# Optimization experiments

Hardware: AMD Instinct MI355X
Metric: run time of the kernel (lower is better)

The kernel has to match this reference:

```python
import jax, jax.numpy as jnp
import numpy as np

D_MODEL = 1024
HEADS = 16
DH = D_MODEL // HEADS
ROPE_THETA = 10000.0


def _rope_cache(T, dh, base, dtype):
    half = dh // 2
    inv_freq = 1.0 / (base ** (jnp.arange(half, dtype=dtype) / half))
    t = jnp.arange(T, dtype=dtype)
    freqs = jnp.outer(t, inv_freq)  # [T, half]
    return jnp.sin(freqs), jnp.cos(freqs)


def _apply_rope(x, sin, cos):
    # x: [B, h, T, dh]; sin/cos: [T, dh//2] broadcast over B,h
    half = sin.shape[-1]
    x1, x2 = x[..., :half], x[..., half:2 * half]
    return jnp.concatenate([x1 * cos - x2 * sin, x1 * sin + x2 * cos], axis=-1)


def setup_inputs() -> dict:
    key = jax.random.key(0)
    ks = jax.random.split(key, 5)
    B, T, D = 4, 2048, D_MODEL
    scale = 1.0 / np.sqrt(D)
    x_btd = jax.random.normal(ks[0], (B, T, D), dtype=jnp.float32)
    Wqkv = jax.random.normal(ks[1], (D, 3 * D), dtype=jnp.float32) * scale
    bqkv = jnp.zeros((3 * D,), dtype=jnp.float32)
    Wproj = jax.random.normal(ks[2], (D, D), dtype=jnp.float32) * scale
    bproj = jnp.zeros((D,), dtype=jnp.float32)
    return {"x_btd": x_btd, "Wqkv": Wqkv, "bqkv": bqkv, "Wproj": Wproj, "bproj": bproj}


def reference(x_btd, Wqkv, bqkv, Wproj, bproj):
    B, T, D = x_btd.shape
    h, dh = HEADS, DH
    qkv = x_btd @ Wqkv + bqkv                      # [B, T, 3D]
    q, k, v = jnp.split(qkv, 3, axis=-1)

    def to_heads(z):
        return z.reshape(B, T, h, dh).transpose(0, 2, 1, 3)  # [B, h, T, dh]

    qh, kh, vh = to_heads(q), to_heads(k), to_heads(v)
    sin, cos = _rope_cache(T, dh, ROPE_THETA, x_btd.dtype)
    qh = _apply_rope(qh, sin, cos)
    kh = _apply_rope(kh, sin, cos)

    scores = jnp.einsum('bhqd,bhkd->bhqk', qh, kh) / jnp.sqrt(jnp.asarray(dh, x_btd.dtype))
    attn = jax.nn.softmax(scores, axis=-1)
    out = jnp.einsum('bhqk,bhkd->bhqd', attn, vh)  # [B, h, T, dh]
    out = out.transpose(0, 2, 1, 3).reshape(B, T, D)
    return out @ Wproj + bproj
```

## Files before the change

kernel.cpp:

```cpp
#include <hip/hip_runtime.h>
#include <stdint.h>


typedef float  f32x4  __attribute__((ext_vector_type(4)));
typedef float  f32x16 __attribute__((ext_vector_type(16)));
typedef short  s16x8  __attribute__((ext_vector_type(8)));
typedef unsigned int u32x4 __attribute__((ext_vector_type(4)));
typedef unsigned short u16;
typedef unsigned int   u32;

#define LOG2E 1.4426950408889634f

__device__ __forceinline__ u16 f2bf(float f) {
  u32 u = __float_as_uint(f);
  u32 r = (u + 0x7fffu + ((u >> 16) & 1u)) >> 16;
  return (u16)r;
}

__device__ __forceinline__ u32 cvtpk_bf16(float lo, float hi) {
  u32 w;
  asm("v_cvt_pk_bf16_f32 %0, %1, %2" : "=v"(w) : "v"(lo), "v"(hi));
  return w;
}

__device__ __forceinline__ float fexp2(float x) {
  return __builtin_amdgcn_exp2f(x);
}

__device__ __forceinline__ void gload_lds16(const u16* g, u16* l) {
  __builtin_amdgcn_global_load_lds(
      (const __attribute__((address_space(1))) uint32_t*)g,
      (__attribute__((address_space(3))) uint32_t*)l, 16, 0, 0);
}

__global__ void rope_table_kernel(float* __restrict__ rsin, float* __restrict__ rcos) {
  int idx = blockIdx.x * 256 + threadIdx.x;
  int t = idx >> 5, i = idx & 31;
  float invf = 1.0f / powf(10000.0f, (float)i * (1.0f / 32.0f));
  float ang = (float)t * invf;
  rsin[idx] = sinf(ang);
  rcos[idx] = cosf(ang);
}

__global__ void cvt_bf16_kernel(const float* __restrict__ in, u16* __restrict__ out) {
  int i = blockIdx.x * 256 + threadIdx.x;
  const float4* p = reinterpret_cast<const float4*>(in) + (size_t)i * 2;
  float4 a = p[0], b = p[1];
  u32 w0 = (u32)f2bf(a.x) | ((u32)f2bf(a.y) << 16);
  u32 w1 = (u32)f2bf(a.z) | ((u32)f2bf(a.w) << 16);
  u32 w2 = (u32)f2bf(b.x) | ((u32)f2bf(b.y) << 16);
  u32 w3 = (u32)f2bf(b.z) | ((u32)f2bf(b.w) << 16);
  reinterpret_cast<uint4*>(out)[i] = make_uint4(w0, w1, w2, w3);
}

__global__ void transpose_cvt_kernel(const float* __restrict__ W, u16* __restrict__ Wt,
                                     int rows , int cols ) {
  __shared__ float tile[32][33];
  int k0 = blockIdx.y * 32, n0 = blockIdx.x * 32;
  int t = threadIdx.x;
  int c = t & 31, r0 = t >> 5;
  #pragma unroll
  for (int i = 0; i < 4; i++) {
    int r = r0 + i * 8;
    tile[r][c] = W[(size_t)(k0 + r) * cols + n0 + c];
  }
  __syncthreads();
  int kk = t & 31, nn0 = t >> 5;
  #pragma unroll
  for (int i = 0; i < 4; i++) {
    int nn = nn0 + i * 8;
    Wt[(size_t)(n0 + nn) * rows + k0 + kk] = f2bf(tile[kk][nn]);
  }
}

template<int MODE>
__global__ __launch_bounds__(256) void gemm_kernel(
    const u16* __restrict__ A, const u16* __restrict__ Bt,
    const float* __restrict__ bias,
    const float* __restrict__ rsin, const float* __restrict__ rcos,
    u16* __restrict__ Qg, u16* __restrict__ Kg, u16* __restrict__ Vtg,
    float* __restrict__ Cout, int K)
{
  __shared__ alignas(16) u16 As[128][64];
  __shared__ alignas(16) u16 Bs[128][64];
  int tid = threadIdx.x;
  int lane = tid & 63, wid = tid >> 6;
  int wr = wid >> 1, wc = wid & 1;
  int l15 = lane & 15, lg = lane >> 4;
  int row0 = blockIdx.x * 128, col0 = blockIdx.y * 128;

  f32x4 acc[4][4] = {};

  int sr = lane >> 3, sc = lane & 7;
  int scol = (sc ^ sr) * 8;
  const u16* asrc = A  + (size_t)(row0 + wid * 32 + sr) * K + scol;
  const u16* bsrc = Bt + (size_t)(col0 + wid * 32 + sr) * K + scol;
  u16* aLds = &As[0][0] + wid * 2048;
  u16* bLds = &Bs[0][0] + wid * 2048;

  for (int k0 = 0; k0 < K; k0 += 64) {
    #pragma unroll
    for (int i = 0; i < 4; i++) {
      gload_lds16(asrc + (size_t)(i * 8) * K + k0, aLds + i * 512);
      gload_lds16(bsrc + (size_t)(i * 8) * K + k0, bLds + i * 512);
    }
    __syncthreads();
    #pragma unroll
    for (int kk = 0; kk < 2; kk++) {
      s16x8 af[4], bf[4];
      #pragma unroll
      for (int m = 0; m < 4; m++) {
        int row = wr * 64 + m * 16 + l15;
        int slot = (kk * 4 + lg) ^ (l15 & 7);
        af[m] = *reinterpret_cast<const s16x8*>(&As[row][slot * 8]);
      }
      #pragma unroll
      for (int n = 0; n < 4; n++) {
        int row = wc * 64 + n * 16 + l15;
        int slot = (kk * 4 + lg) ^ (l15 & 7);
        bf[n] = *reinterpret_cast<const s16x8*>(&Bs[row][slot * 8]);
      }
      #pragma unroll
      for (int m = 0; m < 4; m++)
        #pragma unroll
        for (int n = 0; n < 4; n++)
          acc[m][n] = __builtin_amdgcn_mfma_f32_16x16x32_bf16(af[m], bf[n], acc[m][n], 0, 0, 0);
    }
    __syncthreads();
  }

  if (MODE == 0) {
    int wavecol = col0 + wc * 64;
    int sec = wavecol >> 10;
    int h = (wavecol & 1023) >> 6;
    #pragma unroll
    for (int m = 0; m < 4; m++) {
      int rbase = row0 + wr * 64 + m * 16 + lg * 4;
      if (sec < 2) {
        u16* G = (sec == 0) ? Qg : Kg;
        float qs = (sec == 0) ? 0.125f * LOG2E : 1.0f;
        #pragma unroll
        for (int fc = 0; fc < 2; fc++) {
          int dh = fc * 16 + l15;
          float b1 = bias[wavecol + fc * 16 + l15];
          float b2 = bias[wavecol + fc * 16 + l15 + 32];
          #pragma unroll
          for (int j = 0; j < 4; j++) {
            int grow = rbase + j;
            int bidx = grow >> 11, tt = grow & 2047;
            float sn = rsin[tt * 32 + dh], cs = rcos[tt * 32 + dh];
            float v1 = acc[m][fc][j] + b1;
            float v2 = acc[m][fc + 2][j] + b2;
            float lo = (v1 * cs - v2 * sn) * qs;
            float hi = (v1 * sn + v2 * cs) * qs;
            size_t base = ((size_t)(bidx * 16 + h) * 2048 + tt) * 64;
            G[base + dh]      = f2bf(lo);
            G[base + dh + 32] = f2bf(hi);
          }
        }
      } else {
        #pragma unroll
        for (int fc = 0; fc < 4; fc++) {
          int dh = fc * 16 + l15;
          float bb = bias[wavecol + fc * 16 + l15];
          #pragma unroll
          for (int j = 0; j < 4; j++) {
            int grow = rbase + j;
            int bidx = grow >> 11, tt = grow & 2047;
            Vtg[((size_t)(bidx * 16 + h) * 64 + dh) * 2048 + tt] = f2bf(acc[m][fc][j] + bb);
          }
        }
      }
    }
  } else {
    #pragma unroll
    for (int m = 0; m < 4; m++) {
      int grow = row0 + wr * 64 + m * 16 + lg * 4;
      #pragma unroll
      for (int fc = 0; fc < 4; fc++) {
        int col = col0 + wc * 64 + fc * 16 + l15;
        float bb = bias[col];
        #pragma unroll
        for (int j = 0; j < 4; j++)
          Cout[(size_t)(grow + j) * 1024 + col] = acc[m][fc][j] + bb;
      }
    }
  }
}

__global__ __launch_bounds__(256, 4) void attn_kernel(
    const u16* __restrict__ Qg, const u16* __restrict__ Kg, const u16* __restrict__ Vtg,
    u16* __restrict__ Og)
{
  __shared__ alignas(16) u16 Ks[2][4096];
  __shared__ alignas(16) u16 Vs[2][4096];
  int tid = threadIdx.x;
  int lane = tid & 63, wid = tid >> 6;
  int l31 = lane & 31, hi = lane >> 5;
  int bh = blockIdx.x & 63, qt = blockIdx.x >> 6;
  int q = qt * 128 + wid * 32 + l31;
  size_t bh2048 = (size_t)bh * 2048;

  s16x8 aq[4];
  #pragma unroll
  for (int kc = 0; kc < 4; kc++)
    aq[kc] = *reinterpret_cast<const s16x8*>(Qg + (bh2048 + q) * 64 + kc * 16 + hi * 8);

  f32x16 o0 = {}, o1 = {};
  float l_run = 0.f;

  int sr = lane >> 3, sc = lane & 7;
  int scol = (sc ^ sr) * 8;
  const u16* kg0 = Kg  + (bh2048 + wid * 16 + sr) * 64 + scol;
  const u16* kg1 = kg0 + 8 * 64;
  const u16* vg0 = Vtg + ((size_t)bh * 64 + wid * 16 + sr) * 2048 + scol;
  const u16* vg1 = vg0 + 8 * 2048;
  int sdst = wid * 1024;

  int offs[2][4];
  #pragma unroll
  for (int c = 0; c < 2; c++)
    #pragma unroll
    for (int j = 0; j < 4; j++)
      offs[c][j] = (c * 32 + l31) * 64 + (((j * 2 + hi) ^ (l31 & 7)) * 8);

#define STAGE(TT, BUF) do { \
    gload_lds16(kg0 + (size_t)(TT) * 4096, &Ks[BUF][sdst]); \
    gload_lds16(kg1 + (size_t)(TT) * 4096, &Ks[BUF][sdst + 512]); \
    gload_lds16(vg0 + (size_t)(TT) * 64,   &Vs[BUF][sdst]); \
    gload_lds16(vg1 + (size_t)(TT) * 64,   &Vs[BUF][sdst + 512]); \
  } while (0)

#define COMPUTE(B) do { \
    const u16* kb = &Ks[B][0]; \
    const u16* vb = &Vs[B][0]; \
    f32x16 s0 = {}, s1 = {}; \
    __builtin_amdgcn_s_setprio(1); \
    _Pragma("unroll") \
    for (int j = 0; j < 4; j++) { \
      s16x8 kf0 = *reinterpret_cast<const s16x8*>(kb + offs[0][j]); \
      s16x8 kf1 = *reinterpret_cast<const s16x8*>(kb + offs[1][j]); \
      s0 = __builtin_amdgcn_mfma_f32_32x32x16_bf16(kf0, aq[j], s0, 0, 0, 0); \
      s1 = __builtin_amdgcn_mfma_f32_32x32x16_bf16(kf1, aq[j], s1, 0, 0, 0); \
    } \
    __builtin_amdgcn_s_setprio(0); \
    _Pragma("unroll") \
    for (int i = 0; i < 16; i++) { \
      s0[i] = fexp2(s0[i]); \
      s1[i] = fexp2(s1[i]); \
    } \
    float r0 = 0.f, r1 = 0.f, r2 = 0.f, r3 = 0.f; \
    _Pragma("unroll") \
    for (int i = 0; i < 4; i++) { \
      r0 += s0[i] + s0[i + 8]; \
      r1 += s0[i + 4] + s0[i + 12]; \
      r2 += s1[i] + s1[i + 8]; \
      r3 += s1[i + 4] + s1[i + 12]; \
    } \
    float rs = (r0 + r1) + (r2 + r3); \
    rs += __shfl_xor(rs, 32); \
    l_run += rs; \
    s16x8 pf[4]; \
    _Pragma("unroll") \
    for (int ks = 0; ks < 2; ks++) { \
      int rr = ks * 8; \
      u32 a0 = cvtpk_bf16(s0[rr + 0], s0[rr + 1]); \
      u32 b0 = cvtpk_bf16(s0[rr + 4], s0[rr + 5]); \
      u32 a1 = cvtpk_bf16(s0[rr + 2], s0[rr + 3]); \
      u32 b1 = cvtpk_bf16(s0[rr + 6], s0[rr + 7]); \
      asm volatile("v_permlane32_swap_b32 %0, %1" : "+v"(a0), "+v"(b0)); \
      asm volatile("v_permlane32_swap_b32 %0, %1" : "+v"(a1), "+v"(b1)); \
      u32x4 w = {a0, a1, b0, b1}; \
      pf[ks] = __builtin_bit_cast(s16x8, w); \
    } \
    _Pragma("unroll") \
    for (int ks = 0; ks < 2; ks++) { \
      int rr = ks * 8; \
      u32 a0 = cvtpk_bf16(s1[rr + 0], s1[rr + 1]); \
      u32 b0 = cvtpk_bf16(s1[rr + 4], s1[rr + 5]); \
      u32 a1 = cvtpk_bf16(s1[rr + 2], s1[rr + 3]); \
      u32 b1 = cvtpk_bf16(s1[rr + 6], s1[rr + 7]); \
      asm volatile("v_permlane32_swap_b32 %0, %1" : "+v"(a0), "+v"(b0)); \
      asm volatile("v_permlane32_swap_b32 %0, %1" : "+v"(a1), "+v"(b1)); \
      u32x4 w = {a0, a1, b0, b1}; \
      pf[ks + 2] = __builtin_bit_cast(s16x8, w); \
    } \
    __builtin_amdgcn_s_setprio(1); \
    _Pragma("unroll") \
    for (int ks = 0; ks < 4; ks++) { \
      s16x8 vf = *reinterpret_cast<const s16x8*>(vb + offs[0][ks]); \
      o0 = __builtin_amdgcn_mfma_f32_32x32x16_bf16(vf, pf[ks], o0, 0, 0, 0); \
    } \
    _Pragma("unroll") \
    for (int ks = 0; ks < 4; ks++) { \
      s16x8 vf = *reinterpret_cast<const s16x8*>(vb + offs[1][ks]); \
      o1 = __builtin_amdgcn_mfma_f32_32x32x16_bf16(vf, pf[ks], o1, 0, 0, 0); \
    } \
    __builtin_amdgcn_s_setprio(0); \
  } while (0)

  STAGE(0, 0);
  __syncthreads();

  for (int it = 0; it < 16; it++) {
    STAGE(2 * it + 1, 1);
    COMPUTE(0);
    __syncthreads();
    if (it < 15) STAGE(2 * it + 2, 0);
    COMPUTE(1);
    __syncthreads();
  }
#undef STAGE
#undef COMPUTE

  float inv = 1.0f / l_run;
  int b = bh >> 4, h = bh & 15;
  size_t rowbase = ((size_t)b * 2048 + q) * 1024 + h * 64;
  #pragma unroll
  for (int c2 = 0; c2 < 2; c2++) {
    #pragma unroll
    for (int g = 0; g < 4; g++) {
      float e0 = (c2 ? o1[g * 4 + 0] : o0[g * 4 + 0]) * inv;
      float e1 = (c2 ? o1[g * 4 + 1] : o0[g * 4 + 1]) * inv;
      float e2 = (c2 ? o1[g * 4 + 2] : o0[g * 4 + 2]) * inv;
      float e3 = (c2 ? o1[g * 4 + 3] : o0[g * 4 + 3]) * inv;
      u32 w0 = cvtpk_bf16(e0, e1);
      u32 w1 = cvtpk_bf16(e2, e3);
      int d = c2 * 32 + g * 8 + hi * 4;
      uint2 val; val.x = w0; val.y = w1;
      *reinterpret_cast<uint2*>(Og + rowbase + d) = val;
    }
  }
}

extern "C" void kernel_launch(void* const* d_in, const int* in_sizes, int n_in,
                              void* d_out, int out_size, void* d_ws, size_t ws_size,
                              hipStream_t stream) {
  const float* x     = (const float*)d_in[0];
  const float* Wqkv  = (const float*)d_in[1];
  const float* bqkv  = (const float*)d_in[2];
  const float* Wproj = (const float*)d_in[3];
  const float* bproj = (const float*)d_in[4];
  float* out = (float*)d_out;

  char* ws = (char*)d_ws;
  size_t off = 0;
  auto alloc = [&](size_t bytes) {
    void* p = ws + off;
    off += (bytes + 255) & ~(size_t)255;
    return p;
  };
  float* rsin  = (float*)alloc((size_t)2048 * 32 * 4);
  float* rcos  = (float*)alloc((size_t)2048 * 32 * 4);
  u16* xb      = (u16*)alloc((size_t)8192 * 1024 * 2);
  u16* Wqkvt   = (u16*)alloc((size_t)3072 * 1024 * 2);
  u16* Wprojt  = (u16*)alloc((size_t)1024 * 1024 * 2);
  u16* Qg      = (u16*)alloc((size_t)64 * 2048 * 64 * 2);
  u16* Kg      = (u16*)alloc((size_t)64 * 2048 * 64 * 2);
  u16* Vtg     = (u16*)alloc((size_t)64 * 2048 * 64 * 2);
  u16* AOg     = (u16*)alloc((size_t)8192 * 1024 * 2);

  rope_table_kernel<<<256, 256, 0, stream>>>(rsin, rcos);
  cvt_bf16_kernel<<<4096, 256, 0, stream>>>(x, xb);
  transpose_cvt_kernel<<<dim3(96, 32), 256, 0, stream>>>(Wqkv, Wqkvt, 1024, 3072);
  transpose_cvt_kernel<<<dim3(32, 32), 256, 0, stream>>>(Wproj, Wprojt, 1024, 1024);
  gemm_kernel<0><<<dim3(64, 24), 256, 0, stream>>>(xb, Wqkvt, bqkv, rsin, rcos,
                                                   Qg, Kg, Vtg, nullptr, 1024);
  attn_kernel<<<1024, 256, 0, stream>>>(Qg, Kg, Vtg, AOg);
  gemm_kernel<1><<<dim3(64, 8), 256, 0, stream>>>(AOg, Wprojt, bproj, nullptr, nullptr,
                                                  nullptr, nullptr, nullptr, out, 1024);
}
```

Baseline: 201.1 us.

## Add 256x256-tile 8-wave QKV GEMM with double-buffered direct-to-LDS loads

Adds a new QKV projection GEMM kernel that uses 256x256 output tiles, 512 threads and 128 KB of dynamic LDS. It double-buffers the K tiles with direct global-to-LDS loads, interleaves the prefetch with the MFMA phases, and raises wave priority around the MFMAs. The aim is more operand reuse per LDS byte and overlap of memory with compute. The epilogue moves into a shared helper. The launch falls back to the old kernel if the LDS attribute cannot be set, and the grid of 384 blocks is small enough that some CUs may sit idle.

```diff
diff --git a/kernel.cpp b/kernel.cpp
--- a/kernel.cpp
+++ b/kernel.cpp
@@ -70,6 +70,50 @@
   for (int i = 0; i < 4; i++) {
     int nn = nn0 + i * 8;
     Wt[(size_t)(n0 + nn) * rows + k0 + kk] = f2bf(tile[kk][nn]);
+  }
+}
+
+__device__ __forceinline__ void qkv_scatter_frag(
+    int wavecol, int rbase, int l15, f32x4* accm ,
+    const float* bias, const float* rsin, const float* rcos,
+    u16* Qg, u16* Kg, u16* Vtg)
+{
+  int sec = wavecol >> 10;
+  int h = (wavecol & 1023) >> 6;
+  if (sec < 2) {
+    u16* G = (sec == 0) ? Qg : Kg;
+    float qs = (sec == 0) ? 0.125f * LOG2E : 1.0f;
+    #pragma unroll
+    for (int fc = 0; fc < 2; fc++) {
+      int dh = fc * 16 + l15;
+      float b1 = bias[wavecol + fc * 16 + l15];
+      float b2 = bias[wavecol + fc * 16 + l15 + 32];
+      #pragma unroll
+      for (int j = 0; j < 4; j++) {
+        int grow = rbase + j;
+        int bidx = grow >> 11, tt = grow & 2047;
+        float sn = rsin[tt * 32 + dh], cs = rcos[tt * 32 + dh];
+        float v1 = accm[fc][j] + b1;
+        float v2 = accm[fc + 2][j] + b2;
+        float lo = (v1 * cs - v2 * sn) * qs;
+        float hi = (v1 * sn + v2 * cs) * qs;
+        size_t base = ((size_t)(bidx * 16 + h) * 2048 + tt) * 64;
+        G[base + dh]      = f2bf(lo);
+        G[base + dh + 32] = f2bf(hi);
+      }
+    }
+  } else {
+    #pragma unroll
+    for (int fc = 0; fc < 4; fc++) {
+      int dh = fc * 16 + l15;
+      float bb = bias[wavecol + fc * 16 + l15];
+      #pragma unroll
+      for (int j = 0; j < 4; j++) {
+        int grow = rbase + j;
+        int bidx = grow >> 11, tt = grow & 2047;
+        Vtg[((size_t)(bidx * 16 + h) * 64 + dh) * 2048 + tt] = f2bf(accm[fc][j] + bb);
+      }
+    }
   }
 }
 
@@ -131,51 +175,115 @@
 
   if (MODE == 0) {
     int wavecol = col0 + wc * 64;
-    int sec = wavecol >> 10;
-    int h = (wavecol & 1023) >> 6;
     #pragma unroll
     for (int m = 0; m < 4; m++) {
       int rbase = row0 + wr * 64 + m * 16 + lg * 4;
-      if (sec < 2) {
-        u16* G = (sec == 0) ? Qg : Kg;
-        float qs = (sec == 0) ? 0.125f * LOG2E : 1.0f;
-        #pragma unroll
-        for (int fc = 0; fc < 2; fc++) {
-          int dh = fc * 16 + l15;
-          float b1 = bias[wavecol + fc * 16 + l15];
-          float b2 = bias[wavecol + fc * 16 + l15 + 32];
-          #pragma unroll
-          for (int j = 0; j < 4; j++) {
-            int grow = rbase + j;
-            int bidx = grow >> 11, tt = grow & 2047;
-            float sn = rsin[tt * 32 + dh], cs = rcos[tt * 32 + dh];
-            float v1 = acc[m][fc][j] + b1;
-            float v2 = acc[m][fc + 2][j] + b2;
-            float lo = (v1 * cs - v2 * sn) * qs;
-            float hi = (v1 * sn + v2 * cs) * qs;
-            size_t base = ((size_t)(bidx * 16 + h) * 2048 + tt) * 64;
-            G[base + dh]      = f2bf(lo);
-            G[base + dh + 32] = f2bf(hi);
-          }
-        }
-      } else {
-        #pragma unroll
-        for (int fc = 0; fc < 4; fc++) {
-          int dh = fc * 16 + l15;
-          float bb = bias[wavecol + fc * 16 + l15];
-          #pragma unroll
-          for (int j = 0; j < 4; j++) {
-            int grow = rbase + j;
-            int bidx = grow >> 11, tt = grow & 2047;
-            Vtg[((size_t)(bidx * 16 + h) * 64 + dh) * 2048 + tt] = f2bf(acc[m][fc][j] + bb);
-          }
-        }
-      }
+      qkv_scatter_frag(wavecol, rbase, l15, acc[m], bias, rsin, rcos, Qg, Kg, Vtg);
     }
   } else {
     #pragma unroll
     for (int m = 0; m < 4; m++) {
       int grow = row0 + wr * 64 + m * 16 + lg * 4;
+      #pragma unroll
+      for (int fc = 0; fc < 4; fc++) {
+        int col = col0 + wc * 64 + fc * 16 + l15;
+        float bb = bias[col];
+        #pragma unroll
+        for (int j = 0; j < 4; j++)
+          Cout[(size_t)(grow + j) * 1024 + col] = acc[m][fc][j] + bb;
+      }
+    }
+  }
+}
+
+template<int MODE>
+__global__ __launch_bounds__(512, 2) void gemm8_kernel(
+    const u16* __restrict__ A, const u16* __restrict__ Bt,
+    const float* __restrict__ bias,
+    const float* __restrict__ rsin, const float* __restrict__ rcos,
+    u16* __restrict__ Qg, u16* __restrict__ Kg, u16* __restrict__ Vtg,
+    float* __restrict__ Cout, int K)
+{
+  extern __shared__ u16 lds[];
+  int tid = threadIdx.x;
+  int lane = tid & 63, wid = tid >> 6;
+  int wr = wid >> 2, wc = wid & 3;
+  int l15 = lane & 15, lg = lane >> 4;
+  int row0 = blockIdx.x * 256, col0 = blockIdx.y * 256;
+
+  f32x4 acc[8][4] = {};
+
+  int sr = lane >> 3, sc = lane & 7;
+  int scol = (sc ^ sr) * 8;
+  const u16* asrc = A  + (size_t)(row0 + wid * 32 + sr) * K + scol;
+  const u16* bsrc = Bt + (size_t)(col0 + wid * 32 + sr) * K + scol;
+
+  #pragma unroll
+  for (int i = 0; i < 4; i++) {
+    gload_lds16(asrc + (size_t)(i * 8) * K, lds + wid * 2048 + i * 512);
+    gload_lds16(bsrc + (size_t)(i * 8) * K, lds + 16384 + wid * 2048 + i * 512);
+  }
+  asm volatile("s_waitcnt vmcnt(0)");
+  __builtin_amdgcn_s_barrier();
+
+  const int nt = K >> 6;
+  for (int g = 0; g < nt; ++g) {
+    int b = g & 1;
+    const u16* aB = lds + b * 32768;
+    const u16* bB = lds + b * 32768 + 16384;
+    u16* aD = lds + (b ^ 1) * 32768 + wid * 2048;
+    u16* bD = lds + (b ^ 1) * 32768 + 16384 + wid * 2048;
+    size_t kn = (size_t)(g + 1) << 6;
+    bool pre = (g + 1 < nt);
+
+    #pragma unroll
+    for (int p = 0; p < 4; p++) {
+      const int kk = p >> 1, mh = p & 1;
+      s16x8 af[4], bf[4];
+      #pragma unroll
+      for (int m = 0; m < 4; m++) {
+        int row = wr * 128 + (mh * 4 + m) * 16 + l15;
+        int slot = (kk * 4 + lg) ^ (l15 & 7);
+        af[m] = *reinterpret_cast<const s16x8*>(aB + row * 64 + slot * 8);
+      }
+      #pragma unroll
+      for (int n = 0; n < 4; n++) {
+        int row = wc * 64 + n * 16 + l15;
+        int slot = (kk * 4 + lg) ^ (l15 & 7);
+        bf[n] = *reinterpret_cast<const s16x8*>(bB + row * 64 + slot * 8);
+      }
+      if (pre) {
+        gload_lds16(asrc + (size_t)(p * 8) * K + kn, aD + p * 512);
+        gload_lds16(bsrc + (size_t)(p * 8) * K + kn, bD + p * 512);
+      }
+      __builtin_amdgcn_s_barrier();
+      __builtin_amdgcn_s_setprio(1);
+      #pragma unroll
+      for (int m = 0; m < 4; m++)
+        #pragma unroll
+        for (int n = 0; n < 4; n++)
+          acc[mh * 4 + m][n] =
+              __builtin_amdgcn_mfma_f32_16x16x32_bf16(af[m], bf[n], acc[mh * 4 + m][n], 0, 0, 0);
+      __builtin_amdgcn_s_setprio(0);
+      __builtin_amdgcn_s_barrier();
+    }
+    if (pre) {
+      asm volatile("s_waitcnt vmcnt(0)");
+      __builtin_amdgcn_s_barrier();
+    }
+  }
+
+  if (MODE == 0) {
+    int wavecol = col0 + wc * 64;
+    #pragma unroll
+    for (int m = 0; m < 8; m++) {
+      int rbase = row0 + wr * 128 + m * 16 + lg * 4;
+      qkv_scatter_frag(wavecol, rbase, l15, acc[m], bias, rsin, rcos, Qg, Kg, Vtg);
+    }
+  } else {
+    #pragma unroll
+    for (int m = 0; m < 8; m++) {
+      int grow = row0 + wr * 128 + m * 16 + lg * 4;
       #pragma unroll
       for (int fc = 0; fc < 4; fc++) {
         int col = col0 + wc * 64 + fc * 16 + l15;
@@ -364,8 +472,18 @@
   cvt_bf16_kernel<<<4096, 256, 0, stream>>>(x, xb);
   transpose_cvt_kernel<<<dim3(96, 32), 256, 0, stream>>>(Wqkv, Wqkvt, 1024, 3072);
   transpose_cvt_kernel<<<dim3(32, 32), 256, 0, stream>>>(Wproj, Wprojt, 1024, 1024);
-  gemm_kernel<0><<<dim3(64, 24), 256, 0, stream>>>(xb, Wqkvt, bqkv, rsin, rcos,
-                                                   Qg, Kg, Vtg, nullptr, 1024);
+
+  hipError_t lds_ok = hipFuncSetAttribute(
+      reinterpret_cast<const void*>(&gemm8_kernel<0>),
+      hipFuncAttributeMaxDynamicSharedMemorySize, 131072);
+  if (lds_ok == hipSuccess) {
+    gemm8_kernel<0><<<dim3(32, 12), 512, 131072, stream>>>(
+        xb, Wqkvt, bqkv, rsin, rcos, Qg, Kg, Vtg, nullptr, 1024);
+  } else {
+    gemm_kernel<0><<<dim3(64, 24), 256, 0, stream>>>(
+        xb, Wqkvt, bqkv, rsin, rcos, Qg, Kg, Vtg, nullptr, 1024);
+  }
+
   attn_kernel<<<1024, 256, 0, stream>>>(Qg, Kg, Vtg, AOg);
   gemm_kernel<1><<<dim3(64, 8), 256, 0, stream>>>(AOg, Wprojt, bproj, nullptr, nullptr,
                                                   nullptr, nullptr, nullptr, out, 1024);
```

After: 204.9 us. No clear change (+1.9%).
